# Kernel tuning notes

Measured on AMD Instinct MI355X. Metric: run time of the kernel, lower is better.

## Reference

```python
import jax, jax.numpy as jnp
import numpy as np
import math

WH, WW = 8, 8
N = WH * WW            # tokens per window = 64
DIM = 128
H = 4                  # num_heads
HD = DIM // H          # head_dim = 32
B_ = 3072              # num_windows * batch
NW = 192               # windows per image (96/8 * 128/8)
LAMBDA_INIT = 0.8 - 0.6 * math.exp(-0.3 * 0)  # layer_idx = 0 -> 0.2
EPS_RMS = 1e-9


def _polar_input():
    # Polar-coordinate relative positions, as in __init__
    gy, gx = jnp.meshgrid(jnp.arange(WH), jnp.arange(WW), indexing='ij')
    flat = jnp.stack([gy.reshape(-1), gx.reshape(-1)])          # (2, N)
    rel = flat[:, :, None] - flat[:, None, :]                   # (2, N, N)
    dx = rel[1].astype(jnp.float32)
    dy = -rel[0].astype(jnp.float32)
    r = jnp.sqrt(dx * dx + dy * dy + 1e-9)
    theta = jnp.arctan2(dx, dy)
    max_r = math.sqrt((WH - 1) ** 2 + (WW - 1) ** 2)
    return jnp.stack([r / max_r, (theta + math.pi) / (2 * math.pi)], axis=-1)  # (N, N, 2)


def setup_inputs() -> dict:
    key = jax.random.key(0)
    ks = jax.random.split(key, 16)
    s = 0.02
    inp = {}
    inp['x'] = jax.random.normal(ks[0], (B_, N, DIM), jnp.float32)
    inp['mask'] = jnp.zeros((NW, N, N), jnp.float32)
    inp['Wqkv'] = jax.random.normal(ks[1], (3 * DIM, DIM), jnp.float32) * s
    inp['bqkv'] = jnp.zeros((3 * DIM,), jnp.float32)
    inp['Wqkv2'] = jax.random.normal(ks[2], (2 * DIM, DIM), jnp.float32) * s
    inp['bqkv2'] = jnp.zeros((2 * DIM,), jnp.float32)
    inp['Wp1'] = jax.random.normal(ks[3], (64, 2), jnp.float32) * 0.1
    inp['bp1'] = jnp.zeros((64,), jnp.float32)
    inp['Wp2'] = jax.random.normal(ks[4], (H, 64), jnp.float32) * 0.1
    inp['bp2'] = jnp.zeros((H,), jnp.float32)
    inp['lambda_q1'] = jax.random.normal(ks[5], (HD // 2,), jnp.float32) * 0.1
    inp['lambda_k1'] = jax.random.normal(ks[6], (HD // 2,), jnp.float32) * 0.1
    inp['lambda_q2'] = jax.random.normal(ks[7], (HD // 2,), jnp.float32) * 0.1
    inp['lambda_k2'] = jax.random.normal(ks[8], (HD // 2,), jnp.float32) * 0.1
    inp['subln_w'] = jnp.ones((HD,), jnp.float32)
    inp['Wproj'] = jax.random.normal(ks[9], (DIM, DIM), jnp.float32) * s
    inp['bproj'] = jnp.zeros((DIM,), jnp.float32)
    return inp


def reference(x, mask, Wqkv, bqkv, Wqkv2, bqkv2, Wp1, bp1, Wp2, bp2,
              lambda_q1, lambda_k1, lambda_q2, lambda_k2, subln_w, Wproj, bproj):
    scale = HD ** -0.5
    # primary q, k, v
    qkv = (x @ Wqkv.T + bqkv).reshape(B_, N, 3, H, HD).transpose(2, 0, 3, 1, 4)
    q, k, v = qkv[0] * scale, qkv[1], qkv[2]        # (B_, H, N, HD)
    # secondary q2, k2 for differential attention
    qk2 = (x @ Wqkv2.T + bqkv2).reshape(B_, N, 2, H, HD).transpose(2, 0, 3, 1, 4)
    q2, k2 = qk2[0] * scale, qk2[1]

    attn = jnp.einsum('bhnd,bhmd->bhnm', q, k)      # (B_, H, N, N)
    attn2 = jnp.einsum('bhnd,bhmd->bhnm', q2, k2)

    lam = (jnp.exp(jnp.sum(lambda_q1 * lambda_k1))
           - jnp.exp(jnp.sum(lambda_q2 * lambda_k2)) + LAMBDA_INIT)

    # MLP-based polar relative position bias (exact erf GELU, as nn.GELU)
    pin = _polar_input().reshape(-1, 2)
    pb = jax.nn.gelu(pin @ Wp1.T + bp1, approximate=False) @ Wp2.T + bp2
    pb = pb.reshape(N, N, H).transpose(2, 0, 1)     # (H, N, N)

    attn = attn - lam * attn2 + pb[None]
    # window mask (0 / -inf), broadcast over batch and heads
    attn = attn.reshape(B_ // NW, NW, H, N, N) + mask[None, :, None]
    attn = jax.nn.softmax(attn.reshape(B_, H, N, N), axis=-1)

    o = jnp.einsum('bhnm,bhmd->bhnd', attn, v)      # (B_, H, N, HD)
    # post-attention RMSNorm over head_dim, then differential rescale
    o = o * jax.lax.rsqrt(jnp.mean(o * o, axis=-1, keepdims=True) + EPS_RMS) * subln_w
    o = (o * (1.0 - LAMBDA_INIT)).transpose(0, 2, 1, 3).reshape(B_, N, DIM)
    return o @ Wproj.T + bproj
```

## Files before the change

kernel.cpp:

```cpp
#include <hip/hip_runtime.h>
#include <math.h>

typedef __attribute__((ext_vector_type(8))) short bf16x8;
typedef __attribute__((ext_vector_type(4))) float f32x4;

#define NWMASK 192
#define SCALE_Q 0.17677669529663687f

__device__ __forceinline__ unsigned short f2bf(float f) {
  union { float f; unsigned u; } v; v.f = f;
  return (unsigned short)((v.u + 0x7fffu + ((v.u >> 16) & 1u)) >> 16);
}

__device__ __forceinline__ unsigned pkbf(float a, float b) {
#if defined(__has_builtin)
#if __has_builtin(__builtin_amdgcn_cvt_pk_bf16_f32)
  auto r = __builtin_amdgcn_cvt_pk_bf16_f32(a, b);
  union { decltype(r) v; unsigned u; } c; c.v = r; return c.u;
#else
  return (unsigned)f2bf(a) | ((unsigned)f2bf(b) << 16);
#endif
#else
  return (unsigned)f2bf(a) | ((unsigned)f2bf(b) << 16);
#endif
}

__device__ __forceinline__ void pack8s(unsigned short* dst, const float* src) {
  float4 lo = *(const float4*)(src);
  float4 hi = *(const float4*)(src + 4);
  uint4 pk;
  pk.x = pkbf(lo.x, lo.y); pk.y = pkbf(lo.z, lo.w);
  pk.z = pkbf(hi.x, hi.y); pk.w = pkbf(hi.z, hi.w);
  *(uint4*)dst = pk;
}

__global__ void prep_kernel(const float* __restrict__ Wqkv, const float* __restrict__ Wqkv2,
                            const float* __restrict__ Wproj,
                            const float* __restrict__ Wp1, const float* __restrict__ bp1,
                            const float* __restrict__ Wp2, const float* __restrict__ bp2,
                            const float* __restrict__ mask,
                            unsigned short* __restrict__ Wb, float* __restrict__ pbT,
                            float* __restrict__ maskT) {
  int bid = blockIdx.x;
  if (bid < 48) {
    int gid = bid * 256 + threadIdx.x;
    int l15 = gid & 15, quad = (gid >> 4) & 3, ks = (gid >> 6) & 3, ft = gid >> 8;
    int row = ft * 16 + l15;
    const float* src = (row < 384) ? (Wqkv + (size_t)row * 128)
                     : (row < 640) ? (Wqkv2 + (size_t)(row - 384) * 128)
                                   : (Wproj + (size_t)(row - 640) * 128);
    pack8s(Wb + (size_t)gid * 8, src + ks * 32 + quad * 8);
  } else if (bid < 64) {
    int idx = (bid - 48) * 256 + threadIdx.x;
    int i = idx >> 6, j = idx & 63;
    float dx = (float)((i & 7) - (j & 7));
    float dy = -(float)((i >> 3) - (j >> 3));
    float r = sqrtf(dx*dx + dy*dy + 1e-9f);
    float theta = atan2f(dx, dy);
    float p0 = r * (1.0f / 9.899494936611665f);
    float p1 = (theta + 3.14159265358979323846f) * (1.0f / 6.283185307179586f);
    float a0 = 0.f, a1 = 0.f, a2 = 0.f, a3 = 0.f;
    for (int f = 0; f < 64; ++f) {
      float hpre = p0 * Wp1[2*f] + p1 * Wp1[2*f+1] + bp1[f];
      float g = 0.5f * hpre * (1.0f + erff(hpre * 0.70710678118654752f));
      a0 += Wp2[f]       * g;
      a1 += Wp2[64 + f]  * g;
      a2 += Wp2[128 + f] * g;
      a3 += Wp2[192 + f] * g;
    }
    int o = j * 64 + i;
    pbT[o]          = a0 + bp2[0];
    pbT[4096 + o]   = a1 + bp2[1];
    pbT[8192 + o]   = a2 + bp2[2];
    pbT[12288 + o]  = a3 + bp2[3];
  } else {
    int gid = (bid - 64) * 256 + threadIdx.x;
    int wm = gid >> 12, rc = gid & 4095, c = rc >> 6, r = rc & 63;
    maskT[gid] = mask[(size_t)wm * 4096 + r * 64 + c];
  }
}

__global__ __launch_bounds__(256, 3)
void fused_win(const float* __restrict__ x, const unsigned short* __restrict__ Wb,
               const float* __restrict__ bqkv, const float* __restrict__ bqkv2,
               const float* __restrict__ lq1, const float* __restrict__ lk1,
               const float* __restrict__ lq2, const float* __restrict__ lk2,
               const float* __restrict__ subln, const float* __restrict__ bproj,
               const float* __restrict__ pbT, const float* __restrict__ maskT,
               float* __restrict__ out) {
  __shared__ unsigned short smem[24576];

  const int b = blockIdx.x;
  const int t = threadIdx.x;
  const int w = t >> 6;
  const int lane = t & 63;
  const int l15 = lane & 15;
  const int quad = lane >> 4;
  const int h = w;
  const f32x4 zero4 = (f32x4){0.f, 0.f, 0.f, 0.f};

  {
    const float* xg = x + (size_t)b * 8192;
#pragma unroll
    for (int u = 0; u < 4; ++u) {
      int id = u * 256 + t;
      int r = id >> 4, c16 = id & 15;
      pack8s(&smem[r * 128 + ((c16 ^ (r & 7)) * 8)], xg + r * 128 + c16 * 8);
    }
  }
  __syncthreads();

  float lam;
  {
    float s1 = 0.f, s2 = 0.f;
#pragma unroll
    for (int i = 0; i < 16; ++i) { s1 += lq1[i]*lk1[i]; s2 += lq2[i]*lk2[i]; }
    lam = expf(s1) - expf(s2) + 0.2f;
  }

  unsigned short* PW = smem + 8192 + w * 4096;

  auto ldXB = [&](int mi, int ks) -> bf16x8 {
    int row = mi * 16 + l15;
    return *(const bf16x8*)(&smem[row * 128 + (((ks * 4 + quad) ^ (l15 & 7)) * 8)]);
  };
  auto ldWbF = [&](int ft, int ks) -> bf16x8 {
    return *(const bf16x8*)(Wb + ((((size_t)ft * 4 + ks) * 4 + quad) * 16 + l15) * 8);
  };

  auto proj4 = [&](int ft0, int ft1, int ft2, int ft3, f32x4 acc[4][4]) {
#pragma unroll
    for (int mi = 0; mi < 4; ++mi)
#pragma unroll
      for (int nj = 0; nj < 4; ++nj) acc[mi][nj] = zero4;
#pragma unroll
    for (int ks = 0; ks < 4; ++ks) {
      bf16x8 xa[4], wf[4];
#pragma unroll
      for (int mi = 0; mi < 4; ++mi) xa[mi] = ldXB(mi, ks);
      wf[0] = ldWbF(ft0, ks); wf[1] = ldWbF(ft1, ks);
      wf[2] = ldWbF(ft2, ks); wf[3] = ldWbF(ft3, ks);
#pragma unroll
      for (int mi = 0; mi < 4; ++mi)
#pragma unroll
        for (int nj = 0; nj < 4; ++nj)
          acc[mi][nj] = __builtin_amdgcn_mfma_f32_16x16x32_bf16(xa[mi], wf[nj], acc[mi][nj], 0, 0, 0);
    }
  };
  auto storeQK = [&](f32x4 acc[4][4], const float* biasA, const float* biasB, float scA) {
#pragma unroll
    for (int nj = 0; nj < 4; ++nj) {
      int c32 = (nj & 1) * 16 + l15;
      float bias = (nj < 2) ? biasA[c32] : biasB[c32];
      float sc = (nj < 2) ? scA : 1.0f;
      unsigned short* buf = PW + ((nj < 2) ? 0 : 2048);
#pragma unroll
      for (int mi = 0; mi < 4; ++mi) {
        unsigned p01 = pkbf((acc[mi][nj][0] + bias) * sc, (acc[mi][nj][1] + bias) * sc);
        unsigned p23 = pkbf((acc[mi][nj][2] + bias) * sc, (acc[mi][nj][3] + bias) * sc);
        int r0 = mi * 16 + quad * 4;
        buf[(r0+0) * 32 + (((c32 >> 3) ^ ((r0+0) & 3)) * 8) + (c32 & 7)] = (unsigned short)p01;
        buf[(r0+1) * 32 + (((c32 >> 3) ^ ((r0+1) & 3)) * 8) + (c32 & 7)] = (unsigned short)(p01 >> 16);
        buf[(r0+2) * 32 + (((c32 >> 3) ^ ((r0+2) & 3)) * 8) + (c32 & 7)] = (unsigned short)p23;
        buf[(r0+3) * 32 + (((c32 >> 3) ^ ((r0+3) & 3)) * 8) + (c32 & 7)] = (unsigned short)(p23 >> 16);
      }
    }
  };
  auto qkTiles = [&](f32x4 S[4][4], bool seedBias) {
    bf16x8 qa[4], kb[4];
#pragma unroll
    for (int mi = 0; mi < 4; ++mi) {
      int row = mi * 16 + l15;
      qa[mi] = *(const bf16x8*)(&PW[row * 32 + ((quad ^ (l15 & 3)) * 8)]);
      kb[mi] = *(const bf16x8*)(&PW[2048 + row * 32 + ((quad ^ (l15 & 3)) * 8)]);
    }
    const float* pbh = pbT + h * 4096;
    const float* mkh = maskT + (size_t)(b % NWMASK) * 4096;
#pragma unroll
    for (int mi = 0; mi < 4; ++mi)
#pragma unroll
      for (int ni = 0; ni < 4; ++ni) {
        f32x4 c;
        if (seedBias) {
          int off = (ni * 16 + l15) * 64 + mi * 16 + quad * 4;
          float4 p4 = *(const float4*)(pbh + off);
          float4 m4 = *(const float4*)(mkh + off);
          c[0] = p4.x + m4.x; c[1] = p4.y + m4.y;
          c[2] = p4.z + m4.z; c[3] = p4.w + m4.w;
        } else c = S[mi][ni];
        S[mi][ni] = __builtin_amdgcn_mfma_f32_16x16x32_bf16(qa[mi], kb[ni], c, 0, 0, 0);
      }
  };

  f32x4 S[4][4];
  {
    f32x4 acc[4][4];
    proj4(24 + 2*h, 25 + 2*h, 32 + 2*h, 33 + 2*h, acc);
    storeQK(acc, bqkv2 + h*32, bqkv2 + 128 + h*32, -lam * SCALE_Q);
    qkTiles(S, true);
  }
  {
    f32x4 acc[4][4];
    proj4(2*h, 1 + 2*h, 8 + 2*h, 9 + 2*h, acc);
    storeQK(acc, bqkv + h*32, bqkv + 128 + h*32, SCALE_Q);
    qkTiles(S, false);
  }

#pragma unroll
  for (int mi = 0; mi < 4; ++mi) {
#pragma unroll
    for (int reg = 0; reg < 4; ++reg) {
      float e0 = __expf(S[mi][0][reg]);
      float e1 = __expf(S[mi][1][reg]);
      float e2 = __expf(S[mi][2][reg]);
      float e3 = __expf(S[mi][3][reg]);
      int row = mi * 16 + quad * 4 + reg;
      int sw = row & 7;
      unsigned short* prow = PW + row * 64;
      unsigned p01 = pkbf(e0, e1);
      unsigned p23 = pkbf(e2, e3);
      prow[(((l15 >> 3) + 0) ^ sw) * 8 + (l15 & 7)] = (unsigned short)p01;
      prow[(((l15 >> 3) + 2) ^ sw) * 8 + (l15 & 7)] = (unsigned short)(p01 >> 16);
      prow[(((l15 >> 3) + 4) ^ sw) * 8 + (l15 & 7)] = (unsigned short)p23;
      prow[(((l15 >> 3) + 6) ^ sw) * 8 + (l15 & 7)] = (unsigned short)(p23 >> 16);
    }
  }

  f32x4 av[4][2];
  {
#pragma unroll
    for (int mi = 0; mi < 4; ++mi) { av[mi][0] = zero4; av[mi][1] = zero4; }
#pragma unroll
    for (int ks = 0; ks < 4; ++ks) {
      bf16x8 xa[4];
#pragma unroll
      for (int mi = 0; mi < 4; ++mi) xa[mi] = ldXB(mi, ks);
      bf16x8 w0 = ldWbF(16 + 2*h, ks), w1 = ldWbF(17 + 2*h, ks);
#pragma unroll
      for (int mi = 0; mi < 4; ++mi) {
        av[mi][0] = __builtin_amdgcn_mfma_f32_16x16x32_bf16(xa[mi], w0, av[mi][0], 0, 0, 0);
        av[mi][1] = __builtin_amdgcn_mfma_f32_16x16x32_bf16(xa[mi], w1, av[mi][1], 0, 0, 0);
      }
    }
  }
  __syncthreads();

  {
    unsigned short* VT = smem + w * 2048;
#pragma unroll
    for (int nd = 0; nd < 2; ++nd) {
      int d = nd * 16 + l15;
      float bias = bqkv[256 + h * 32 + d];
#pragma unroll
      for (int mi = 0; mi < 4; ++mi) {
        int tok0 = mi * 16 + quad * 4;
        uint2 pk;
        pk.x = pkbf(av[mi][nd][0] + bias, av[mi][nd][1] + bias);
        pk.y = pkbf(av[mi][nd][2] + bias, av[mi][nd][3] + bias);
        *(uint2*)(&VT[d * 64 + (((tok0 >> 3) ^ (d & 7)) * 8) + (tok0 & 7)]) = pk;
      }
    }
  }

  float ov0[4][4], ov1[4][4];
  {
    unsigned short* VT = smem + w * 2048;
    f32x4 O[4][2];
#pragma unroll
    for (int mi = 0; mi < 4; ++mi) { O[mi][0] = zero4; O[mi][1] = zero4; }
#pragma unroll
    for (int kc = 0; kc < 2; ++kc) {
      bf16x8 pa[4], vb[2];
#pragma unroll
      for (int mi = 0; mi < 4; ++mi) {
        int row = mi * 16 + l15;
        pa[mi] = *(const bf16x8*)(&PW[row * 64 + (((kc * 4 + quad) ^ (row & 7)) * 8)]);
      }
#pragma unroll
      for (int nd = 0; nd < 2; ++nd) {
        int d = nd * 16 + l15;
        vb[nd] = *(const bf16x8*)(&VT[d * 64 + (((kc * 4 + quad) ^ (d & 7)) * 8)]);
      }
#pragma unroll
      for (int mi = 0; mi < 4; ++mi) {
        O[mi][0] = __builtin_amdgcn_mfma_f32_16x16x32_bf16(pa[mi], vb[0], O[mi][0], 0, 0, 0);
        O[mi][1] = __builtin_amdgcn_mfma_f32_16x16x32_bf16(pa[mi], vb[1], O[mi][1], 0, 0, 0);
      }
    }
    float sw0 = subln[l15] * 0.8f;
    float sw1 = subln[16 + l15] * 0.8f;
#pragma unroll
    for (int mi = 0; mi < 4; ++mi)
#pragma unroll
      for (int reg = 0; reg < 4; ++reg) {
        float a0 = O[mi][0][reg], a1 = O[mi][1][reg];
        float ss = a0 * a0 + a1 * a1;
        ss += __shfl_xor(ss, 1);
        ss += __shfl_xor(ss, 2);
        ss += __shfl_xor(ss, 4);
        ss += __shfl_xor(ss, 8);
        float rs = 1.0f / sqrtf(ss * (1.0f / 32.0f));
        ov0[mi][reg] = a0 * rs * sw0;
        ov1[mi][reg] = a1 * rs * sw1;
      }
  }

  __syncthreads();

  {
    int c0 = h * 32 + l15, c1 = h * 32 + 16 + l15;
#pragma unroll
    for (int mi = 0; mi < 4; ++mi)
#pragma unroll
      for (int reg = 0; reg < 4; ++reg) {
        int row = mi * 16 + quad * 4 + reg;
        unsigned short* orow = smem + 8192 + row * 128;
        unsigned p = pkbf(ov0[mi][reg], ov1[mi][reg]);
        orow[(((c0 >> 3) ^ (row & 7)) * 8) + (c0 & 7)] = (unsigned short)p;
        orow[(((c1 >> 3) ^ (row & 7)) * 8) + (c1 & 7)] = (unsigned short)(p >> 16);
      }
  }
  __syncthreads();

  {
    f32x4 po[4][2];
#pragma unroll
    for (int mi = 0; mi < 4; ++mi) { po[mi][0] = zero4; po[mi][1] = zero4; }
#pragma unroll
    for (int ks = 0; ks < 4; ++ks) {
      bf16x8 oa[4];
#pragma unroll
      for (int mi = 0; mi < 4; ++mi) {
        int row = mi * 16 + l15;
        oa[mi] = *(const bf16x8*)(&smem[8192 + row * 128 + (((ks * 4 + quad) ^ (l15 & 7)) * 8)]);
      }
      bf16x8 w0 = ldWbF(40 + 2*w, ks), w1 = ldWbF(41 + 2*w, ks);
#pragma unroll
      for (int mi = 0; mi < 4; ++mi) {
        po[mi][0] = __builtin_amdgcn_mfma_f32_16x16x32_bf16(oa[mi], w0, po[mi][0], 0, 0, 0);
        po[mi][1] = __builtin_amdgcn_mfma_f32_16x16x32_bf16(oa[mi], w1, po[mi][1], 0, 0, 0);
      }
    }
    float* og = out + (size_t)b * 8192;
#pragma unroll
    for (int nt = 0; nt < 2; ++nt) {
      int col = (2 * w + nt) * 16 + l15;
      float bp = bproj[col];
#pragma unroll
      for (int mi = 0; mi < 4; ++mi)
#pragma unroll
        for (int reg = 0; reg < 4; ++reg)
          og[(size_t)(mi * 16 + quad * 4 + reg) * 128 + col] = po[mi][nt][reg] + bp;
    }
  }
}

extern "C" void kernel_launch(void* const* d_in, const int* in_sizes, int n_in,
                              void* d_out, int out_size, void* d_ws, size_t ws_size,
                              hipStream_t stream) {
  (void)in_sizes; (void)n_in; (void)out_size; (void)ws_size;
  const float* x     = (const float*)d_in[0];
  const float* mask  = (const float*)d_in[1];
  const float* Wqkv  = (const float*)d_in[2];
  const float* bqkv  = (const float*)d_in[3];
  const float* Wqkv2 = (const float*)d_in[4];
  const float* bqkv2 = (const float*)d_in[5];
  const float* Wp1   = (const float*)d_in[6];
  const float* bp1   = (const float*)d_in[7];
  const float* Wp2   = (const float*)d_in[8];
  const float* bp2   = (const float*)d_in[9];
  const float* lq1   = (const float*)d_in[10];
  const float* lk1   = (const float*)d_in[11];
  const float* lq2   = (const float*)d_in[12];
  const float* lk2   = (const float*)d_in[13];
  const float* subln = (const float*)d_in[14];
  const float* Wproj = (const float*)d_in[15];
  const float* bproj = (const float*)d_in[16];
  float* out = (float*)d_out;

  unsigned short* Wb = (unsigned short*)d_ws;
  float* pbT   = (float*)((char*)d_ws + 262144);
  float* maskT = (float*)((char*)d_ws + 327680);

  hipLaunchKernelGGL(prep_kernel, dim3(3136), dim3(256), 0, stream,
                     Wqkv, Wqkv2, Wproj, Wp1, bp1, Wp2, bp2, mask, Wb, pbT, maskT);
  hipLaunchKernelGGL(fused_win, dim3(3072), dim3(256), 0, stream,
                     x, Wb, bqkv, bqkv2, lq1, lk1, lq2, lk2, subln, bproj,
                     pbT, maskT, out);
}
```

Baseline: 312.9 us.

## Shrink LDS to 32KB for 4 blocks/CU, read x from global, split P store

The fused window kernel no longer stages x in shared memory. Each projection now loads x straight from global memory and converts it to bf16 per fragment. The P matrix is written in two 32-column halves that reuse the Q buffer, with V^T placed in the K buffer, which cuts LDS from 48KB to 32KB and raises launch bounds to 4 blocks per CU. Lambda is computed once in the prep kernel, the mask transpose uses a coalesced LDS tile with one block per window, and s_setprio brackets are placed around the MFMA bursts. The cost is that x is now read from global or L2 several times per block (once per projection pass) instead of once, and register pressure is tighter under the new launch bound.

```diff
diff --git a/kernel.cpp b/kernel.cpp
--- a/kernel.cpp
+++ b/kernel.cpp
@@ -39,8 +39,10 @@
                             const float* __restrict__ Wp1, const float* __restrict__ bp1,
                             const float* __restrict__ Wp2, const float* __restrict__ bp2,
                             const float* __restrict__ mask,
+                            const float* __restrict__ lq1, const float* __restrict__ lk1,
+                            const float* __restrict__ lq2, const float* __restrict__ lk2,
                             unsigned short* __restrict__ Wb, float* __restrict__ pbT,
-                            float* __restrict__ maskT) {
+                            float* __restrict__ maskT, float* __restrict__ lamOut) {
   int bid = blockIdx.x;
   if (bid < 48) {
     int gid = bid * 256 + threadIdx.x;
@@ -73,22 +75,43 @@
     pbT[4096 + o]   = a1 + bp2[1];
     pbT[8192 + o]   = a2 + bp2[2];
     pbT[12288 + o]  = a3 + bp2[3];
+    if (bid == 48 && threadIdx.x == 0) {
+      float s1 = 0.f, s2 = 0.f;
+      for (int k = 0; k < 16; ++k) { s1 += lq1[k]*lk1[k]; s2 += lq2[k]*lk2[k]; }
+      lamOut[0] = expf(s1) - expf(s2) + 0.2f;
+    }
   } else {
-    int gid = (bid - 64) * 256 + threadIdx.x;
-    int wm = gid >> 12, rc = gid & 4095, c = rc >> 6, r = rc & 63;
-    maskT[gid] = mask[(size_t)wm * 4096 + r * 64 + c];
-  }
-}
-
-__global__ __launch_bounds__(256, 3)
+    __shared__ float tile[64][65];
+    int wm = bid - 64;
+    const float* src = mask + (size_t)wm * 4096;
+#pragma unroll
+    for (int u = 0; u < 4; ++u) {
+      int o = u * 1024 + threadIdx.x * 4;
+      float4 v = *(const float4*)(src + o);
+      int r = o >> 6, c = o & 63;
+      tile[r][c] = v.x; tile[r][c+1] = v.y; tile[r][c+2] = v.z; tile[r][c+3] = v.w;
+    }
+    __syncthreads();
+    float* dst = maskT + (size_t)wm * 4096;
+#pragma unroll
+    for (int u = 0; u < 4; ++u) {
+      int o = u * 1024 + threadIdx.x * 4;
+      int c = o >> 6, r = o & 63;
+      float4 v;
+      v.x = tile[r][c]; v.y = tile[r+1][c]; v.z = tile[r+2][c]; v.w = tile[r+3][c];
+      *(float4*)(dst + o) = v;
+    }
+  }
+}
+
+__global__ __launch_bounds__(256, 4)
 void fused_win(const float* __restrict__ x, const unsigned short* __restrict__ Wb,
                const float* __restrict__ bqkv, const float* __restrict__ bqkv2,
-               const float* __restrict__ lq1, const float* __restrict__ lk1,
-               const float* __restrict__ lq2, const float* __restrict__ lk2,
+               const float* __restrict__ lamBuf,
                const float* __restrict__ subln, const float* __restrict__ bproj,
                const float* __restrict__ pbT, const float* __restrict__ maskT,
                float* __restrict__ out) {
-  __shared__ unsigned short smem[24576];
+  __shared__ unsigned short smem[16384];
 
   const int b = blockIdx.x;
   const int t = threadIdx.x;
@@ -98,37 +121,25 @@
   const int quad = lane >> 4;
   const int h = w;
   const f32x4 zero4 = (f32x4){0.f, 0.f, 0.f, 0.f};
-
-  {
-    const float* xg = x + (size_t)b * 8192;
-#pragma unroll
-    for (int u = 0; u < 4; ++u) {
-      int id = u * 256 + t;
-      int r = id >> 4, c16 = id & 15;
-      pack8s(&smem[r * 128 + ((c16 ^ (r & 7)) * 8)], xg + r * 128 + c16 * 8);
-    }
-  }
-  __syncthreads();
-
-  float lam;
-  {
-    float s1 = 0.f, s2 = 0.f;
-#pragma unroll
-    for (int i = 0; i < 16; ++i) { s1 += lq1[i]*lk1[i]; s2 += lq2[i]*lk2[i]; }
-    lam = expf(s1) - expf(s2) + 0.2f;
-  }
-
-  unsigned short* PW = smem + 8192 + w * 4096;
-
-  auto ldXB = [&](int mi, int ks) -> bf16x8 {
-    int row = mi * 16 + l15;
-    return *(const bf16x8*)(&smem[row * 128 + (((ks * 4 + quad) ^ (l15 & 7)) * 8)]);
+  const float lam = lamBuf[0];
+  const float* xg = x + (size_t)b * 8192;
+
+  unsigned short* PW = smem + w * 4096;
+
+  auto ldXG = [&](int mi, int ks) -> bf16x8 {
+    const float* p = xg + (size_t)(mi * 16 + l15) * 128 + ks * 32 + quad * 8;
+    float4 lo = *(const float4*)p;
+    float4 hi = *(const float4*)(p + 4);
+    uint4 pk;
+    pk.x = pkbf(lo.x, lo.y); pk.y = pkbf(lo.z, lo.w);
+    pk.z = pkbf(hi.x, hi.y); pk.w = pkbf(hi.z, hi.w);
+    union { uint4 u; bf16x8 v; } cv; cv.u = pk; return cv.v;
   };
   auto ldWbF = [&](int ft, int ks) -> bf16x8 {
     return *(const bf16x8*)(Wb + ((((size_t)ft * 4 + ks) * 4 + quad) * 16 + l15) * 8);
   };
 
-  auto proj4 = [&](int ft0, int ft1, int ft2, int ft3, f32x4 acc[4][4]) {
+  auto proj4 = [&](int ft0, int ft1, int ft2, int ft3, f32x4 (&acc)[4][4]) {
 #pragma unroll
     for (int mi = 0; mi < 4; ++mi)
 #pragma unroll
@@ -137,27 +148,45 @@
     for (int ks = 0; ks < 4; ++ks) {
       bf16x8 xa[4], wf[4];
 #pragma unroll
-      for (int mi = 0; mi < 4; ++mi) xa[mi] = ldXB(mi, ks);
+      for (int mi = 0; mi < 4; ++mi) xa[mi] = ldXG(mi, ks);
       wf[0] = ldWbF(ft0, ks); wf[1] = ldWbF(ft1, ks);
       wf[2] = ldWbF(ft2, ks); wf[3] = ldWbF(ft3, ks);
+      __builtin_amdgcn_s_setprio(1);
 #pragma unroll
       for (int mi = 0; mi < 4; ++mi)
 #pragma unroll
         for (int nj = 0; nj < 4; ++nj)
           acc[mi][nj] = __builtin_amdgcn_mfma_f32_16x16x32_bf16(xa[mi], wf[nj], acc[mi][nj], 0, 0, 0);
-    }
-  };
-  auto storeQK = [&](f32x4 acc[4][4], const float* biasA, const float* biasB, float scA) {
-#pragma unroll
-    for (int nj = 0; nj < 4; ++nj) {
-      int c32 = (nj & 1) * 16 + l15;
-      float bias = (nj < 2) ? biasA[c32] : biasB[c32];
-      float sc = (nj < 2) ? scA : 1.0f;
-      unsigned short* buf = PW + ((nj < 2) ? 0 : 2048);
-#pragma unroll
-      for (int mi = 0; mi < 4; ++mi) {
-        unsigned p01 = pkbf((acc[mi][nj][0] + bias) * sc, (acc[mi][nj][1] + bias) * sc);
-        unsigned p23 = pkbf((acc[mi][nj][2] + bias) * sc, (acc[mi][nj][3] + bias) * sc);
+      __builtin_amdgcn_s_setprio(0);
+    }
+  };
+  auto proj2 = [&](int ft0, int ft1, f32x4 (&acc)[4][4]) {
+#pragma unroll
+    for (int mi = 0; mi < 4; ++mi) { acc[mi][0] = zero4; acc[mi][1] = zero4; }
+#pragma unroll
+    for (int ks = 0; ks < 4; ++ks) {
+      bf16x8 w0 = ldWbF(ft0, ks), w1 = ldWbF(ft1, ks);
+#pragma unroll
+      for (int mi = 0; mi < 4; ++mi) {
+        bf16x8 xa = ldXG(mi, ks);
+        __builtin_amdgcn_s_setprio(1);
+        acc[mi][0] = __builtin_amdgcn_mfma_f32_16x16x32_bf16(xa, w0, acc[mi][0], 0, 0, 0);
+        acc[mi][1] = __builtin_amdgcn_mfma_f32_16x16x32_bf16(xa, w1, acc[mi][1], 0, 0, 0);
+        __builtin_amdgcn_s_setprio(0);
+      }
+    }
+  };
+  auto storeM = [&](f32x4 (&acc)[4][4], int njo, const float* bias, float sc,
+                    unsigned short* buf) {
+#pragma unroll
+    for (int nj = 0; nj < 2; ++nj) {
+      int c32 = nj * 16 + l15;
+      float bv = bias[c32];
+#pragma unroll
+      for (int mi = 0; mi < 4; ++mi) {
+        f32x4 a = acc[mi][njo + nj];
+        unsigned p01 = pkbf((a[0] + bv) * sc, (a[1] + bv) * sc);
+        unsigned p23 = pkbf((a[2] + bv) * sc, (a[3] + bv) * sc);
         int r0 = mi * 16 + quad * 4;
         buf[(r0+0) * 32 + (((c32 >> 3) ^ ((r0+0) & 3)) * 8) + (c32 & 7)] = (unsigned short)p01;
         buf[(r0+1) * 32 + (((c32 >> 3) ^ ((r0+1) & 3)) * 8) + (c32 & 7)] = (unsigned short)(p01 >> 16);
@@ -166,7 +195,7 @@
       }
     }
   };
-  auto qkTiles = [&](f32x4 S[4][4], bool seedBias) {
+  auto qkTiles = [&](f32x4 (&S)[4][4], bool seedBias) {
     bf16x8 qa[4], kb[4];
 #pragma unroll
     for (int mi = 0; mi < 4; ++mi) {
@@ -176,6 +205,7 @@
     }
     const float* pbh = pbT + h * 4096;
     const float* mkh = maskT + (size_t)(b % NWMASK) * 4096;
+    __builtin_amdgcn_s_setprio(1);
 #pragma unroll
     for (int mi = 0; mi < 4; ++mi)
 #pragma unroll
@@ -190,63 +220,57 @@
         } else c = S[mi][ni];
         S[mi][ni] = __builtin_amdgcn_mfma_f32_16x16x32_bf16(qa[mi], kb[ni], c, 0, 0, 0);
       }
+    __builtin_amdgcn_s_setprio(0);
+  };
+  auto storeHalf = [&](unsigned (&pe)[4][4]) {
+#pragma unroll
+    for (int mi = 0; mi < 4; ++mi)
+#pragma unroll
+      for (int reg = 0; reg < 4; ++reg) {
+        int row = mi * 16 + quad * 4 + reg;
+        unsigned short* prow = PW + row * 32;
+        unsigned v = pe[mi][reg];
+        int sw = row & 3;
+        prow[(((l15 >> 3) + 0) ^ sw) * 8 + (l15 & 7)] = (unsigned short)v;
+        prow[(((l15 >> 3) + 2) ^ sw) * 8 + (l15 & 7)] = (unsigned short)(v >> 16);
+      }
   };
 
   f32x4 S[4][4];
   {
     f32x4 acc[4][4];
     proj4(24 + 2*h, 25 + 2*h, 32 + 2*h, 33 + 2*h, acc);
-    storeQK(acc, bqkv2 + h*32, bqkv2 + 128 + h*32, -lam * SCALE_Q);
+    storeM(acc, 0, bqkv2 + h*32, -lam * SCALE_Q, PW);
+    storeM(acc, 2, bqkv2 + 128 + h*32, 1.0f, PW + 2048);
     qkTiles(S, true);
   }
   {
     f32x4 acc[4][4];
-    proj4(2*h, 1 + 2*h, 8 + 2*h, 9 + 2*h, acc);
-    storeQK(acc, bqkv + h*32, bqkv + 128 + h*32, SCALE_Q);
+    proj2(2*h, 1 + 2*h, acc);
+    storeM(acc, 0, bqkv + h*32, SCALE_Q, PW);
+    proj2(8 + 2*h, 9 + 2*h, acc);
+    storeM(acc, 0, bqkv + 128 + h*32, 1.0f, PW + 2048);
     qkTiles(S, false);
   }
 
-#pragma unroll
-  for (int mi = 0; mi < 4; ++mi) {
+  unsigned pe01[4][4], pe23[4][4];
+#pragma unroll
+  for (int mi = 0; mi < 4; ++mi)
 #pragma unroll
     for (int reg = 0; reg < 4; ++reg) {
       float e0 = __expf(S[mi][0][reg]);
       float e1 = __expf(S[mi][1][reg]);
       float e2 = __expf(S[mi][2][reg]);
       float e3 = __expf(S[mi][3][reg]);
-      int row = mi * 16 + quad * 4 + reg;
-      int sw = row & 7;
-      unsigned short* prow = PW + row * 64;
-      unsigned p01 = pkbf(e0, e1);
-      unsigned p23 = pkbf(e2, e3);
-      prow[(((l15 >> 3) + 0) ^ sw) * 8 + (l15 & 7)] = (unsigned short)p01;
-      prow[(((l15 >> 3) + 2) ^ sw) * 8 + (l15 & 7)] = (unsigned short)(p01 >> 16);
-      prow[(((l15 >> 3) + 4) ^ sw) * 8 + (l15 & 7)] = (unsigned short)p23;
-      prow[(((l15 >> 3) + 6) ^ sw) * 8 + (l15 & 7)] = (unsigned short)(p23 >> 16);
-    }
-  }
-
-  f32x4 av[4][2];
-  {
-#pragma unroll
-    for (int mi = 0; mi < 4; ++mi) { av[mi][0] = zero4; av[mi][1] = zero4; }
-#pragma unroll
-    for (int ks = 0; ks < 4; ++ks) {
-      bf16x8 xa[4];
-#pragma unroll
-      for (int mi = 0; mi < 4; ++mi) xa[mi] = ldXB(mi, ks);
-      bf16x8 w0 = ldWbF(16 + 2*h, ks), w1 = ldWbF(17 + 2*h, ks);
-#pragma unroll
-      for (int mi = 0; mi < 4; ++mi) {
-        av[mi][0] = __builtin_amdgcn_mfma_f32_16x16x32_bf16(xa[mi], w0, av[mi][0], 0, 0, 0);
-        av[mi][1] = __builtin_amdgcn_mfma_f32_16x16x32_bf16(xa[mi], w1, av[mi][1], 0, 0, 0);
-      }
-    }
-  }
-  __syncthreads();
-
-  {
-    unsigned short* VT = smem + w * 2048;
+      pe01[mi][reg] = pkbf(e0, e1);
+      pe23[mi][reg] = pkbf(e2, e3);
+    }
+  storeHalf(pe01);
+
+  {
+    f32x4 av[4][4];
+    proj2(16 + 2*h, 17 + 2*h, av);
+    unsigned short* VT = PW + 2048;
 #pragma unroll
     for (int nd = 0; nd < 2; ++nd) {
       int d = nd * 16 + l15;
@@ -264,28 +288,50 @@
 
   float ov0[4][4], ov1[4][4];
   {
-    unsigned short* VT = smem + w * 2048;
+    unsigned short* VT = PW + 2048;
     f32x4 O[4][2];
 #pragma unroll
     for (int mi = 0; mi < 4; ++mi) { O[mi][0] = zero4; O[mi][1] = zero4; }
-#pragma unroll
-    for (int kc = 0; kc < 2; ++kc) {
+    {
       bf16x8 pa[4], vb[2];
 #pragma unroll
       for (int mi = 0; mi < 4; ++mi) {
         int row = mi * 16 + l15;
-        pa[mi] = *(const bf16x8*)(&PW[row * 64 + (((kc * 4 + quad) ^ (row & 7)) * 8)]);
+        pa[mi] = *(const bf16x8*)(&PW[row * 32 + ((quad ^ (l15 & 3)) * 8)]);
       }
 #pragma unroll
       for (int nd = 0; nd < 2; ++nd) {
         int d = nd * 16 + l15;
-        vb[nd] = *(const bf16x8*)(&VT[d * 64 + (((kc * 4 + quad) ^ (d & 7)) * 8)]);
-      }
+        vb[nd] = *(const bf16x8*)(&VT[d * 64 + ((quad ^ (d & 7)) * 8)]);
+      }
+      __builtin_amdgcn_s_setprio(1);
 #pragma unroll
       for (int mi = 0; mi < 4; ++mi) {
         O[mi][0] = __builtin_amdgcn_mfma_f32_16x16x32_bf16(pa[mi], vb[0], O[mi][0], 0, 0, 0);
         O[mi][1] = __builtin_amdgcn_mfma_f32_16x16x32_bf16(pa[mi], vb[1], O[mi][1], 0, 0, 0);
       }
+      __builtin_amdgcn_s_setprio(0);
+    }
+    storeHalf(pe23);
+    {
+      bf16x8 pa[4], vb[2];
+#pragma unroll
+      for (int mi = 0; mi < 4; ++mi) {
+        int row = mi * 16 + l15;
+        pa[mi] = *(const bf16x8*)(&PW[row * 32 + ((quad ^ (l15 & 3)) * 8)]);
+      }
+#pragma unroll
+      for (int nd = 0; nd < 2; ++nd) {
+        int d = nd * 16 + l15;
+        vb[nd] = *(const bf16x8*)(&VT[d * 64 + (((4 + quad) ^ (d & 7)) * 8)]);
+      }
+      __builtin_amdgcn_s_setprio(1);
+#pragma unroll
+      for (int mi = 0; mi < 4; ++mi) {
+        O[mi][0] = __builtin_amdgcn_mfma_f32_16x16x32_bf16(pa[mi], vb[0], O[mi][0], 0, 0, 0);
+        O[mi][1] = __builtin_amdgcn_mfma_f32_16x16x32_bf16(pa[mi], vb[1], O[mi][1], 0, 0, 0);
+      }
+      __builtin_amdgcn_s_setprio(0);
     }
     float sw0 = subln[l15] * 0.8f;
     float sw1 = subln[16 + l15] * 0.8f;
@@ -314,7 +360,7 @@
 #pragma unroll
       for (int reg = 0; reg < 4; ++reg) {
         int row = mi * 16 + quad * 4 + reg;
-        unsigned short* orow = smem + 8192 + row * 128;
+        unsigned short* orow = smem + row * 128;
         unsigned p = pkbf(ov0[mi][reg], ov1[mi][reg]);
         orow[(((c0 >> 3) ^ (row & 7)) * 8) + (c0 & 7)] = (unsigned short)p;
         orow[(((c1 >> 3) ^ (row & 7)) * 8) + (c1 & 7)] = (unsigned short)(p >> 16);
@@ -332,14 +378,16 @@
 #pragma unroll
       for (int mi = 0; mi < 4; ++mi) {
         int row = mi * 16 + l15;
-        oa[mi] = *(const bf16x8*)(&smem[8192 + row * 128 + (((ks * 4 + quad) ^ (l15 & 7)) * 8)]);
+        oa[mi] = *(const bf16x8*)(&smem[row * 128 + (((ks * 4 + quad) ^ (l15 & 7)) * 8)]);
       }
       bf16x8 w0 = ldWbF(40 + 2*w, ks), w1 = ldWbF(41 + 2*w, ks);
+      __builtin_amdgcn_s_setprio(1);
 #pragma unroll
       for (int mi = 0; mi < 4; ++mi) {
         po[mi][0] = __builtin_amdgcn_mfma_f32_16x16x32_bf16(oa[mi], w0, po[mi][0], 0, 0, 0);
         po[mi][1] = __builtin_amdgcn_mfma_f32_16x16x32_bf16(oa[mi], w1, po[mi][1], 0, 0, 0);
       }
+      __builtin_amdgcn_s_setprio(0);
     }
     float* og = out + (size_t)b * 8192;
 #pragma unroll
@@ -379,12 +427,14 @@
   float* out = (float*)d_out;
 
   unsigned short* Wb = (unsigned short*)d_ws;
+  float* lamBuf = (float*)((char*)d_ws + 200704);
   float* pbT   = (float*)((char*)d_ws + 262144);
   float* maskT = (float*)((char*)d_ws + 327680);
 
-  hipLaunchKernelGGL(prep_kernel, dim3(3136), dim3(256), 0, stream,
-                     Wqkv, Wqkv2, Wproj, Wp1, bp1, Wp2, bp2, mask, Wb, pbT, maskT);
+  hipLaunchKernelGGL(prep_kernel, dim3(256), dim3(256), 0, stream,
+                     Wqkv, Wqkv2, Wproj, Wp1, bp1, Wp2, bp2, mask,
+                     lq1, lk1, lq2, lk2, Wb, pbT, maskT, lamBuf);
   hipLaunchKernelGGL(fused_win, dim3(3072), dim3(256), 0, stream,
-                     x, Wb, bqkv, bqkv2, lq1, lk1, lq2, lk2, subln, bproj,
+                     x, Wb, bqkv, bqkv2, lamBuf, subln, bproj,
                      pbT, maskT, out);
 }
```

Measured after the change: 562.1 us. 79.6% more time.

## Transpose MFMA operand order to drop mask transpose and vectorize stores

Applied to the files above, without the earlier changes.

Swaps the A/B operands of every MFMA so each lane's accumulator holds contiguous columns. This allows packed uint2 stores to LDS, float4 output stores and a cheaper RMSNorm reduction with two shuffles. Because the score layout now matches the original row-major orientation, the prep kernel no longer transposes the 192-window mask, and the mask is read directly. Lambda is computed once in prep, and s_setprio is wrapped around MFMA bursts. The risk is different register pressure and scheduling at 3 waves per SIMD.

```diff
diff --git a/kernel.cpp b/kernel.cpp
--- a/kernel.cpp
+++ b/kernel.cpp
@@ -38,9 +38,10 @@
                             const float* __restrict__ Wproj,
                             const float* __restrict__ Wp1, const float* __restrict__ bp1,
                             const float* __restrict__ Wp2, const float* __restrict__ bp2,
-                            const float* __restrict__ mask,
-                            unsigned short* __restrict__ Wb, float* __restrict__ pbT,
-                            float* __restrict__ maskT) {
+                            const float* __restrict__ lq1, const float* __restrict__ lk1,
+                            const float* __restrict__ lq2, const float* __restrict__ lk2,
+                            unsigned short* __restrict__ Wb, float* __restrict__ pbN,
+                            float* __restrict__ lamOut) {
   int bid = blockIdx.x;
   if (bid < 48) {
     int gid = bid * 256 + threadIdx.x;
@@ -50,7 +51,7 @@
                      : (row < 640) ? (Wqkv2 + (size_t)(row - 384) * 128)
                                    : (Wproj + (size_t)(row - 640) * 128);
     pack8s(Wb + (size_t)gid * 8, src + ks * 32 + quad * 8);
-  } else if (bid < 64) {
+  } else {
     int idx = (bid - 48) * 256 + threadIdx.x;
     int i = idx >> 6, j = idx & 63;
     float dx = (float)((i & 7) - (j & 7));
@@ -68,25 +69,25 @@
       a2 += Wp2[128 + f] * g;
       a3 += Wp2[192 + f] * g;
     }
-    int o = j * 64 + i;
-    pbT[o]          = a0 + bp2[0];
-    pbT[4096 + o]   = a1 + bp2[1];
-    pbT[8192 + o]   = a2 + bp2[2];
-    pbT[12288 + o]  = a3 + bp2[3];
-  } else {
-    int gid = (bid - 64) * 256 + threadIdx.x;
-    int wm = gid >> 12, rc = gid & 4095, c = rc >> 6, r = rc & 63;
-    maskT[gid] = mask[(size_t)wm * 4096 + r * 64 + c];
+    int o = i * 64 + j;
+    pbN[o]          = a0 + bp2[0];
+    pbN[4096 + o]   = a1 + bp2[1];
+    pbN[8192 + o]   = a2 + bp2[2];
+    pbN[12288 + o]  = a3 + bp2[3];
+    if (bid == 48 && threadIdx.x == 0) {
+      float s1 = 0.f, s2 = 0.f;
+      for (int k = 0; k < 16; ++k) { s1 += lq1[k]*lk1[k]; s2 += lq2[k]*lk2[k]; }
+      lamOut[0] = expf(s1) - expf(s2) + 0.2f;
+    }
   }
 }
 
 __global__ __launch_bounds__(256, 3)
 void fused_win(const float* __restrict__ x, const unsigned short* __restrict__ Wb,
                const float* __restrict__ bqkv, const float* __restrict__ bqkv2,
-               const float* __restrict__ lq1, const float* __restrict__ lk1,
-               const float* __restrict__ lq2, const float* __restrict__ lk2,
+               const float* __restrict__ lamBuf,
                const float* __restrict__ subln, const float* __restrict__ bproj,
-               const float* __restrict__ pbT, const float* __restrict__ maskT,
+               const float* __restrict__ pbN, const float* __restrict__ mask,
                float* __restrict__ out) {
   __shared__ unsigned short smem[24576];
 
@@ -98,6 +99,7 @@
   const int quad = lane >> 4;
   const int h = w;
   const f32x4 zero4 = (f32x4){0.f, 0.f, 0.f, 0.f};
+  const float lam = lamBuf[0];
 
   {
     const float* xg = x + (size_t)b * 8192;
@@ -110,15 +112,9 @@
   }
   __syncthreads();
 
-  float lam;
-  {
-    float s1 = 0.f, s2 = 0.f;
-#pragma unroll
-    for (int i = 0; i < 16; ++i) { s1 += lq1[i]*lk1[i]; s2 += lq2[i]*lk2[i]; }
-    lam = expf(s1) - expf(s2) + 0.2f;
-  }
-
   unsigned short* PW = smem + 8192 + w * 4096;
+  unsigned short* QB = PW;
+  unsigned short* KB = PW + 2048;
 
   auto ldXB = [&](int mi, int ks) -> bf16x8 {
     int row = mi * 16 + l15;
@@ -128,11 +124,11 @@
     return *(const bf16x8*)(Wb + ((((size_t)ft * 4 + ks) * 4 + quad) * 16 + l15) * 8);
   };
 
-  auto proj4 = [&](int ft0, int ft1, int ft2, int ft3, f32x4 acc[4][4]) {
-#pragma unroll
-    for (int mi = 0; mi < 4; ++mi)
-#pragma unroll
-      for (int nj = 0; nj < 4; ++nj) acc[mi][nj] = zero4;
+  auto proj4T = [&](int ft0, int ft1, int ft2, int ft3, f32x4 (&acc)[4][4]) {
+#pragma unroll
+    for (int nj = 0; nj < 4; ++nj)
+#pragma unroll
+      for (int mi = 0; mi < 4; ++mi) acc[nj][mi] = zero4;
 #pragma unroll
     for (int ks = 0; ks < 4; ++ks) {
       bf16x8 xa[4], wf[4];
@@ -140,90 +136,91 @@
       for (int mi = 0; mi < 4; ++mi) xa[mi] = ldXB(mi, ks);
       wf[0] = ldWbF(ft0, ks); wf[1] = ldWbF(ft1, ks);
       wf[2] = ldWbF(ft2, ks); wf[3] = ldWbF(ft3, ks);
-#pragma unroll
-      for (int mi = 0; mi < 4; ++mi)
-#pragma unroll
-        for (int nj = 0; nj < 4; ++nj)
-          acc[mi][nj] = __builtin_amdgcn_mfma_f32_16x16x32_bf16(xa[mi], wf[nj], acc[mi][nj], 0, 0, 0);
+      __builtin_amdgcn_s_setprio(1);
+#pragma unroll
+      for (int nj = 0; nj < 4; ++nj)
+#pragma unroll
+        for (int mi = 0; mi < 4; ++mi)
+          acc[nj][mi] = __builtin_amdgcn_mfma_f32_16x16x32_bf16(wf[nj], xa[mi], acc[nj][mi], 0, 0, 0);
+      __builtin_amdgcn_s_setprio(0);
     }
   };
-  auto storeQK = [&](f32x4 acc[4][4], const float* biasA, const float* biasB, float scA) {
+  auto storeQKT = [&](f32x4 (&acc)[4][4], const float* biasA, const float* biasB, float scA) {
 #pragma unroll
     for (int nj = 0; nj < 4; ++nj) {
-      int c32 = (nj & 1) * 16 + l15;
-      float bias = (nj < 2) ? biasA[c32] : biasB[c32];
+      int njl = nj & 1;
+      unsigned short* buf = (nj < 2) ? QB : KB;
+      const float* bs = (nj < 2) ? biasA : biasB;
       float sc = (nj < 2) ? scA : 1.0f;
-      unsigned short* buf = PW + ((nj < 2) ? 0 : 2048);
-#pragma unroll
-      for (int mi = 0; mi < 4; ++mi) {
-        unsigned p01 = pkbf((acc[mi][nj][0] + bias) * sc, (acc[mi][nj][1] + bias) * sc);
-        unsigned p23 = pkbf((acc[mi][nj][2] + bias) * sc, (acc[mi][nj][3] + bias) * sc);
-        int r0 = mi * 16 + quad * 4;
-        buf[(r0+0) * 32 + (((c32 >> 3) ^ ((r0+0) & 3)) * 8) + (c32 & 7)] = (unsigned short)p01;
-        buf[(r0+1) * 32 + (((c32 >> 3) ^ ((r0+1) & 3)) * 8) + (c32 & 7)] = (unsigned short)(p01 >> 16);
-        buf[(r0+2) * 32 + (((c32 >> 3) ^ ((r0+2) & 3)) * 8) + (c32 & 7)] = (unsigned short)p23;
-        buf[(r0+3) * 32 + (((c32 >> 3) ^ ((r0+3) & 3)) * 8) + (c32 & 7)] = (unsigned short)(p23 >> 16);
+      float4 bv = *(const float4*)(bs + njl * 16 + quad * 4);
+      int g = njl * 2 + (quad >> 1);
+      int d7 = (quad & 1) * 4;
+#pragma unroll
+      for (int mi = 0; mi < 4; ++mi) {
+        f32x4 a = acc[nj][mi];
+        uint2 pk;
+        pk.x = pkbf((a[0] + bv.x) * sc, (a[1] + bv.y) * sc);
+        pk.y = pkbf((a[2] + bv.z) * sc, (a[3] + bv.w) * sc);
+        int tok = mi * 16 + l15;
+        *(uint2*)(&buf[tok * 32 + ((g ^ (tok & 3)) * 8) + d7]) = pk;
       }
     }
   };
-  auto qkTiles = [&](f32x4 S[4][4], bool seedBias) {
+  auto qkAllT = [&](f32x4 (&S)[4][4], bool seed) {
     bf16x8 qa[4], kb[4];
 #pragma unroll
-    for (int mi = 0; mi < 4; ++mi) {
-      int row = mi * 16 + l15;
-      qa[mi] = *(const bf16x8*)(&PW[row * 32 + ((quad ^ (l15 & 3)) * 8)]);
-      kb[mi] = *(const bf16x8*)(&PW[2048 + row * 32 + ((quad ^ (l15 & 3)) * 8)]);
-    }
-    const float* pbh = pbT + h * 4096;
-    const float* mkh = maskT + (size_t)(b % NWMASK) * 4096;
-#pragma unroll
-    for (int mi = 0; mi < 4; ++mi)
-#pragma unroll
-      for (int ni = 0; ni < 4; ++ni) {
+    for (int i = 0; i < 4; ++i) {
+      int row = i * 16 + l15;
+      qa[i] = *(const bf16x8*)(&QB[row * 32 + ((quad ^ (row & 3)) * 8)]);
+      kb[i] = *(const bf16x8*)(&KB[row * 32 + ((quad ^ (row & 3)) * 8)]);
+    }
+    const float* pbh = pbN + h * 4096;
+    const float* mkh = mask + (size_t)(b % NWMASK) * 4096;
+    __builtin_amdgcn_s_setprio(1);
+#pragma unroll
+    for (int kt = 0; kt < 4; ++kt)
+#pragma unroll
+      for (int qt = 0; qt < 4; ++qt) {
         f32x4 c;
-        if (seedBias) {
-          int off = (ni * 16 + l15) * 64 + mi * 16 + quad * 4;
+        if (seed) {
+          int off = (qt * 16 + l15) * 64 + kt * 16 + quad * 4;
           float4 p4 = *(const float4*)(pbh + off);
           float4 m4 = *(const float4*)(mkh + off);
           c[0] = p4.x + m4.x; c[1] = p4.y + m4.y;
           c[2] = p4.z + m4.z; c[3] = p4.w + m4.w;
-        } else c = S[mi][ni];
-        S[mi][ni] = __builtin_amdgcn_mfma_f32_16x16x32_bf16(qa[mi], kb[ni], c, 0, 0, 0);
-      }
+        } else c = S[kt][qt];
+        S[kt][qt] = __builtin_amdgcn_mfma_f32_16x16x32_bf16(kb[kt], qa[qt], c, 0, 0, 0);
+      }
+    __builtin_amdgcn_s_setprio(0);
   };
 
   f32x4 S[4][4];
   {
     f32x4 acc[4][4];
-    proj4(24 + 2*h, 25 + 2*h, 32 + 2*h, 33 + 2*h, acc);
-    storeQK(acc, bqkv2 + h*32, bqkv2 + 128 + h*32, -lam * SCALE_Q);
-    qkTiles(S, true);
+    proj4T(24 + 2*h, 25 + 2*h, 32 + 2*h, 33 + 2*h, acc);
+    storeQKT(acc, bqkv2 + h*32, bqkv2 + 128 + h*32, -lam * SCALE_Q);
+    qkAllT(S, true);
   }
   {
     f32x4 acc[4][4];
-    proj4(2*h, 1 + 2*h, 8 + 2*h, 9 + 2*h, acc);
-    storeQK(acc, bqkv + h*32, bqkv + 128 + h*32, SCALE_Q);
-    qkTiles(S, false);
-  }
-
-#pragma unroll
-  for (int mi = 0; mi < 4; ++mi) {
-#pragma unroll
-    for (int reg = 0; reg < 4; ++reg) {
-      float e0 = __expf(S[mi][0][reg]);
-      float e1 = __expf(S[mi][1][reg]);
-      float e2 = __expf(S[mi][2][reg]);
-      float e3 = __expf(S[mi][3][reg]);
-      int row = mi * 16 + quad * 4 + reg;
-      int sw = row & 7;
-      unsigned short* prow = PW + row * 64;
-      unsigned p01 = pkbf(e0, e1);
-      unsigned p23 = pkbf(e2, e3);
-      prow[(((l15 >> 3) + 0) ^ sw) * 8 + (l15 & 7)] = (unsigned short)p01;
-      prow[(((l15 >> 3) + 2) ^ sw) * 8 + (l15 & 7)] = (unsigned short)(p01 >> 16);
-      prow[(((l15 >> 3) + 4) ^ sw) * 8 + (l15 & 7)] = (unsigned short)p23;
-      prow[(((l15 >> 3) + 6) ^ sw) * 8 + (l15 & 7)] = (unsigned short)(p23 >> 16);
-    }
+    proj4T(2*h, 1 + 2*h, 8 + 2*h, 9 + 2*h, acc);
+    storeQKT(acc, bqkv + h*32, bqkv + 128 + h*32, SCALE_Q);
+    qkAllT(S, false);
+  }
+
+  {
+    int d7 = (quad & 1) * 4;
+#pragma unroll
+    for (int kt = 0; kt < 4; ++kt)
+#pragma unroll
+      for (int qt = 0; qt < 4; ++qt) {
+        uint2 pk;
+        pk.x = pkbf(__expf(S[kt][qt][0]), __expf(S[kt][qt][1]));
+        pk.y = pkbf(__expf(S[kt][qt][2]), __expf(S[kt][qt][3]));
+        int q = qt * 16 + l15;
+        int g = kt * 2 + (quad >> 1);
+        *(uint2*)(&PW[q * 64 + ((g ^ (q & 7)) * 8) + d7]) = pk;
+      }
   }
 
   f32x4 av[4][2];
@@ -236,121 +233,138 @@
 #pragma unroll
       for (int mi = 0; mi < 4; ++mi) xa[mi] = ldXB(mi, ks);
       bf16x8 w0 = ldWbF(16 + 2*h, ks), w1 = ldWbF(17 + 2*h, ks);
+      __builtin_amdgcn_s_setprio(1);
 #pragma unroll
       for (int mi = 0; mi < 4; ++mi) {
         av[mi][0] = __builtin_amdgcn_mfma_f32_16x16x32_bf16(xa[mi], w0, av[mi][0], 0, 0, 0);
         av[mi][1] = __builtin_amdgcn_mfma_f32_16x16x32_bf16(xa[mi], w1, av[mi][1], 0, 0, 0);
       }
+      __builtin_amdgcn_s_setprio(0);
     }
   }
   __syncthreads();
 
-  {
-    unsigned short* VT = smem + w * 2048;
+  unsigned short* VT = smem + w * 2048;
+  {
+    const float* vbias = bqkv + 256 + h * 32;
 #pragma unroll
     for (int nd = 0; nd < 2; ++nd) {
       int d = nd * 16 + l15;
-      float bias = bqkv[256 + h * 32 + d];
+      float bv = vbias[d];
 #pragma unroll
       for (int mi = 0; mi < 4; ++mi) {
         int tok0 = mi * 16 + quad * 4;
         uint2 pk;
-        pk.x = pkbf(av[mi][nd][0] + bias, av[mi][nd][1] + bias);
-        pk.y = pkbf(av[mi][nd][2] + bias, av[mi][nd][3] + bias);
+        pk.x = pkbf(av[mi][nd][0] + bv, av[mi][nd][1] + bv);
+        pk.y = pkbf(av[mi][nd][2] + bv, av[mi][nd][3] + bv);
         *(uint2*)(&VT[d * 64 + (((tok0 >> 3) ^ (d & 7)) * 8) + (tok0 & 7)]) = pk;
       }
     }
   }
 
-  float ov0[4][4], ov1[4][4];
-  {
-    unsigned short* VT = smem + w * 2048;
-    f32x4 O[4][2];
-#pragma unroll
-    for (int mi = 0; mi < 4; ++mi) { O[mi][0] = zero4; O[mi][1] = zero4; }
+  f32x4 O[2][4];
+  {
+#pragma unroll
+    for (int dt = 0; dt < 2; ++dt)
+#pragma unroll
+      for (int qt = 0; qt < 4; ++qt) O[dt][qt] = zero4;
 #pragma unroll
     for (int kc = 0; kc < 2; ++kc) {
-      bf16x8 pa[4], vb[2];
-#pragma unroll
-      for (int mi = 0; mi < 4; ++mi) {
-        int row = mi * 16 + l15;
-        pa[mi] = *(const bf16x8*)(&PW[row * 64 + (((kc * 4 + quad) ^ (row & 7)) * 8)]);
-      }
-#pragma unroll
-      for (int nd = 0; nd < 2; ++nd) {
-        int d = nd * 16 + l15;
-        vb[nd] = *(const bf16x8*)(&VT[d * 64 + (((kc * 4 + quad) ^ (d & 7)) * 8)]);
-      }
-#pragma unroll
-      for (int mi = 0; mi < 4; ++mi) {
-        O[mi][0] = __builtin_amdgcn_mfma_f32_16x16x32_bf16(pa[mi], vb[0], O[mi][0], 0, 0, 0);
-        O[mi][1] = __builtin_amdgcn_mfma_f32_16x16x32_bf16(pa[mi], vb[1], O[mi][1], 0, 0, 0);
-      }
-    }
-    float sw0 = subln[l15] * 0.8f;
-    float sw1 = subln[16 + l15] * 0.8f;
-#pragma unroll
-    for (int mi = 0; mi < 4; ++mi)
-#pragma unroll
-      for (int reg = 0; reg < 4; ++reg) {
-        float a0 = O[mi][0][reg], a1 = O[mi][1][reg];
-        float ss = a0 * a0 + a1 * a1;
-        ss += __shfl_xor(ss, 1);
-        ss += __shfl_xor(ss, 2);
-        ss += __shfl_xor(ss, 4);
-        ss += __shfl_xor(ss, 8);
-        float rs = 1.0f / sqrtf(ss * (1.0f / 32.0f));
-        ov0[mi][reg] = a0 * rs * sw0;
-        ov1[mi][reg] = a1 * rs * sw1;
-      }
-  }
-
+      bf16x8 vb[2], pa[4];
+#pragma unroll
+      for (int dt = 0; dt < 2; ++dt) {
+        int d = dt * 16 + l15;
+        vb[dt] = *(const bf16x8*)(&VT[d * 64 + (((kc * 4 + quad) ^ (d & 7)) * 8)]);
+      }
+#pragma unroll
+      for (int qt = 0; qt < 4; ++qt) {
+        int q = qt * 16 + l15;
+        pa[qt] = *(const bf16x8*)(&PW[q * 64 + (((kc * 4 + quad) ^ (q & 7)) * 8)]);
+      }
+      __builtin_amdgcn_s_setprio(1);
+#pragma unroll
+      for (int dt = 0; dt < 2; ++dt)
+#pragma unroll
+        for (int qt = 0; qt < 4; ++qt)
+          O[dt][qt] = __builtin_amdgcn_mfma_f32_16x16x32_bf16(vb[dt], pa[qt], O[dt][qt], 0, 0, 0);
+      __builtin_amdgcn_s_setprio(0);
+    }
+    float4 s0 = *(const float4*)(subln + quad * 4);
+    float4 s1 = *(const float4*)(subln + 16 + quad * 4);
+    s0.x *= 0.8f; s0.y *= 0.8f; s0.z *= 0.8f; s0.w *= 0.8f;
+    s1.x *= 0.8f; s1.y *= 0.8f; s1.z *= 0.8f; s1.w *= 0.8f;
+#pragma unroll
+    for (int qt = 0; qt < 4; ++qt) {
+      float ss = 0.f;
+#pragma unroll
+      for (int dt = 0; dt < 2; ++dt)
+#pragma unroll
+        for (int r = 0; r < 4; ++r) ss += O[dt][qt][r] * O[dt][qt][r];
+      ss += __shfl_xor(ss, 16);
+      ss += __shfl_xor(ss, 32);
+      float rs = 1.0f / sqrtf(ss * (1.0f / 32.0f));
+      O[0][qt][0] *= rs * s0.x; O[0][qt][1] *= rs * s0.y;
+      O[0][qt][2] *= rs * s0.z; O[0][qt][3] *= rs * s0.w;
+      O[1][qt][0] *= rs * s1.x; O[1][qt][1] *= rs * s1.y;
+      O[1][qt][2] *= rs * s1.z; O[1][qt][3] *= rs * s1.w;
+    }
+  }
   __syncthreads();
 
-  {
-    int c0 = h * 32 + l15, c1 = h * 32 + 16 + l15;
-#pragma unroll
-    for (int mi = 0; mi < 4; ++mi)
-#pragma unroll
-      for (int reg = 0; reg < 4; ++reg) {
-        int row = mi * 16 + quad * 4 + reg;
-        unsigned short* orow = smem + 8192 + row * 128;
-        unsigned p = pkbf(ov0[mi][reg], ov1[mi][reg]);
-        orow[(((c0 >> 3) ^ (row & 7)) * 8) + (c0 & 7)] = (unsigned short)p;
-        orow[(((c1 >> 3) ^ (row & 7)) * 8) + (c1 & 7)] = (unsigned short)(p >> 16);
+  unsigned short* OB = smem + 8192;
+  {
+    int d7 = (quad & 1) * 4;
+#pragma unroll
+    for (int qt = 0; qt < 4; ++qt)
+#pragma unroll
+      for (int dt = 0; dt < 2; ++dt) {
+        int q = qt * 16 + l15;
+        int c0 = h * 32 + dt * 16 + quad * 4;
+        int g = c0 >> 3;
+        uint2 pk;
+        pk.x = pkbf(O[dt][qt][0], O[dt][qt][1]);
+        pk.y = pkbf(O[dt][qt][2], O[dt][qt][3]);
+        *(uint2*)(&OB[q * 128 + ((g ^ (q & 7)) * 8) + d7]) = pk;
       }
   }
   __syncthreads();
 
   {
-    f32x4 po[4][2];
-#pragma unroll
-    for (int mi = 0; mi < 4; ++mi) { po[mi][0] = zero4; po[mi][1] = zero4; }
+    f32x4 po[2][4];
+#pragma unroll
+    for (int nt = 0; nt < 2; ++nt)
+#pragma unroll
+      for (int mi = 0; mi < 4; ++mi) po[nt][mi] = zero4;
 #pragma unroll
     for (int ks = 0; ks < 4; ++ks) {
       bf16x8 oa[4];
 #pragma unroll
       for (int mi = 0; mi < 4; ++mi) {
         int row = mi * 16 + l15;
-        oa[mi] = *(const bf16x8*)(&smem[8192 + row * 128 + (((ks * 4 + quad) ^ (l15 & 7)) * 8)]);
+        oa[mi] = *(const bf16x8*)(&OB[row * 128 + (((ks * 4 + quad) ^ (l15 & 7)) * 8)]);
       }
       bf16x8 w0 = ldWbF(40 + 2*w, ks), w1 = ldWbF(41 + 2*w, ks);
-#pragma unroll
-      for (int mi = 0; mi < 4; ++mi) {
-        po[mi][0] = __builtin_amdgcn_mfma_f32_16x16x32_bf16(oa[mi], w0, po[mi][0], 0, 0, 0);
-        po[mi][1] = __builtin_amdgcn_mfma_f32_16x16x32_bf16(oa[mi], w1, po[mi][1], 0, 0, 0);
-      }
+      __builtin_amdgcn_s_setprio(1);
+#pragma unroll
+      for (int mi = 0; mi < 4; ++mi) {
+        po[0][mi] = __builtin_amdgcn_mfma_f32_16x16x32_bf16(w0, oa[mi], po[0][mi], 0, 0, 0);
+        po[1][mi] = __builtin_amdgcn_mfma_f32_16x16x32_bf16(w1, oa[mi], po[1][mi], 0, 0, 0);
+      }
+      __builtin_amdgcn_s_setprio(0);
     }
     float* og = out + (size_t)b * 8192;
 #pragma unroll
     for (int nt = 0; nt < 2; ++nt) {
-      int col = (2 * w + nt) * 16 + l15;
-      float bp = bproj[col];
-#pragma unroll
-      for (int mi = 0; mi < 4; ++mi)
-#pragma unroll
-        for (int reg = 0; reg < 4; ++reg)
-          og[(size_t)(mi * 16 + quad * 4 + reg) * 128 + col] = po[mi][nt][reg] + bp;
+      int oc = (2 * w + nt) * 16 + quad * 4;
+      float4 bp = *(const float4*)(bproj + oc);
+#pragma unroll
+      for (int mi = 0; mi < 4; ++mi) {
+        int tok = mi * 16 + l15;
+        float4 st;
+        st.x = po[nt][mi][0] + bp.x; st.y = po[nt][mi][1] + bp.y;
+        st.z = po[nt][mi][2] + bp.z; st.w = po[nt][mi][3] + bp.w;
+        *(float4*)(og + (size_t)tok * 128 + oc) = st;
+      }
     }
   }
 }
@@ -379,12 +393,13 @@
   float* out = (float*)d_out;
 
   unsigned short* Wb = (unsigned short*)d_ws;
-  float* pbT   = (float*)((char*)d_ws + 262144);
-  float* maskT = (float*)((char*)d_ws + 327680);
-
-  hipLaunchKernelGGL(prep_kernel, dim3(3136), dim3(256), 0, stream,
-                     Wqkv, Wqkv2, Wproj, Wp1, bp1, Wp2, bp2, mask, Wb, pbT, maskT);
+  float* lamBuf = (float*)((char*)d_ws + 200704);
+  float* pbN    = (float*)((char*)d_ws + 262144);
+
+  hipLaunchKernelGGL(prep_kernel, dim3(64), dim3(256), 0, stream,
+                     Wqkv, Wqkv2, Wproj, Wp1, bp1, Wp2, bp2,
+                     lq1, lk1, lq2, lk2, Wb, pbN, lamBuf);
   hipLaunchKernelGGL(fused_win, dim3(3072), dim3(256), 0, stream,
-                     x, Wb, bqkv, bqkv2, lq1, lk1, lq2, lk2, subln, bproj,
-                     pbT, maskT, out);
-}
+                     x, Wb, bqkv, bqkv2, lamBuf, subln, bproj,
+                     pbN, mask, out);
+}
```

After: 325.5 us. 1.04x slower.
